# Optimization experiments

Measured on AMD Instinct MI355X. Metric: run time of the kernel, lower is better.

Reference implementation:

```python
import jax, jax.numpy as jnp
import numpy as np

B, N, K, DIMS, F_DIMS = 2, 32768, 16, 2, 32
DS, DH, DO = 32, 32, 32
DA = DS + DH                      # 64
CH = (DIMS + 1) * (1 + K) + DIMS  # 53
CONV_IN = DIMS + (1 + K) * DA     # 1090
CONV_OUT = (1 + K) * DO           # 544


def setup_inputs() -> dict:
    key = jax.random.key(0)
    ks = jax.random.split(key, 6)
    s = 0.05
    return {
        "pc": jax.random.normal(ks[0], (B, N, 1 + K, DIMS), jnp.float32),
        "feats": jax.random.normal(ks[1], (B, N, 1 + K, F_DIMS), jnp.float32),
        "W_mlp": jax.random.normal(ks[2], (CH, DS), jnp.float32) * s,
        "b_mlp": jnp.zeros((DS,), jnp.float32),
        "W_att": jax.random.normal(ks[3], (DA, DA), jnp.float32) * s,
        "b_att": jnp.zeros((DA,), jnp.float32),
        "W_conv": jax.random.normal(ks[4], (CONV_IN, CONV_OUT), jnp.float32) * s,
        "b_conv": jnp.zeros((CONV_OUT,), jnp.float32),
        "W_skip": jax.random.normal(ks[5], (DO + F_DIMS, DO), jnp.float32) * s,
        "b_skip": jnp.zeros((DO,), jnp.float32),
    }


def reference(pc, feats, W_mlp, b_mlp, W_att, b_att, W_conv, b_conv, W_skip, b_skip):
    # ---- LocSE: relative-position encoding ----
    # rpbn_i[b,n,j] = concat(pc[b,n,i] - pc[b,n,j], ||pc[b,n,j]||)
    norms = jnp.linalg.norm(pc, axis=-1, keepdims=True)          # (B,N,1+K,1)
    # diffs[b,n,j,i,:] = pc[b,n,i,:] - pc[b,n,j,:]
    diffs = pc[:, :, None, :, :] - pc[:, :, :, None, :]          # (B,N,1+K,1+K,dims)
    norms_b = jnp.broadcast_to(norms[:, :, :, None, :], diffs.shape[:-1] + (1,))
    blocks = jnp.concatenate([diffs, norms_b], axis=-1)          # (B,N,1+K,1+K,dims+1)
    blocks = blocks.reshape(pc.shape[:3] + ((1 + K) * (DIMS + 1),))
    rppe = jnp.concatenate([pc, blocks], axis=-1)                # (B,N,1+K,CH)
    r = jax.nn.relu(rppe @ W_mlp + b_mlp)                        # (B,N,1+K,DS)
    se = jnp.concatenate([r, feats], axis=-1)                    # (B,N,1+K,DA)

    # ---- attention pooling (softmax over channel axis) ----
    att = jax.nn.softmax(se @ W_att + b_att, axis=-1) * se       # (B,N,1+K,DA)
    reshaped = att.reshape(att.shape[0], att.shape[1], (1 + K) * DA)

    cat = jnp.concatenate([pc[:, :, 0], reshaped], axis=-1)      # (B,N,CONV_IN)
    res = jax.nn.relu(cat @ W_conv + b_conv)                     # (B,N,(1+K)*DO)
    res = res.reshape(res.shape[0], res.shape[1], 1 + K, DO)

    skip_in = jnp.concatenate([feats, res], axis=-1)             # (B,N,1+K,F+DO)
    skip = jax.nn.relu(skip_in @ W_skip + b_skip)                # (B,N,1+K,DO)
    return skip
```

## Files before the change

### kernel.cpp

```cpp
#include <hip/hip_runtime.h>
#include <hip/hip_bf16.h>
#include <cstdint>

#define KNB      17
#define CH       53
#define MP       16
#define BM       64
#define NTHR     512
#define NRT      17
#define SE_LD    72
#define CATW     1120
#define RES_LD   552
#define CHUNK_PTS 32768

#define NE_CONV  (35*34*512)
#define NE_MLP   (2*2*512)
#define NE_ATT   (2*4*512)
#define NE_SKIP  (2*2*512)
#define WS_MLP   (NE_CONV)
#define WS_ATT   (WS_MLP + NE_MLP)
#define WS_SKIP  (WS_ATT + NE_ATT)
#define WS_TOTAL (WS_SKIP + NE_SKIP)

typedef __bf16 bf16x8 __attribute__((ext_vector_type(8)));
typedef float  f32x4  __attribute__((ext_vector_type(4)));
typedef unsigned short u16x4 __attribute__((ext_vector_type(4)));
typedef unsigned short u16x8 __attribute__((ext_vector_type(8)));

__device__ __forceinline__ unsigned short f2b(float f) {
    union { __bf16 h; unsigned short u; } v; v.h = (__bf16)f; return v.u;
}
__device__ __forceinline__ float b2f(unsigned short b) {
    union { unsigned u; float f; } v; v.u = ((unsigned)b) << 16;
    return v.f;
}
__device__ __forceinline__ void gload_lds16(const void* g, void* l) {
    __builtin_amdgcn_global_load_lds(
        (const __attribute__((address_space(1))) unsigned int*)g,
        (__attribute__((address_space(3))) unsigned int*)l, 16, 0, 0);
}

__global__ void seac_prep(const float* __restrict__ Wmlp, const float* __restrict__ Watt,
                          const float* __restrict__ Wconv, const float* __restrict__ Wskip,
                          unsigned short* __restrict__ ws)
{
    int i = blockIdx.x * 256 + threadIdx.x;
    if (i >= WS_TOTAL) return;
    float v;
    if (i < WS_MLP) {
        int idx = i;
        int jj = idx & 7, l = (idx >> 3) & 63, t = idx >> 9;
        int nt = t % 34, ks = t / 34;
        int k = 32*ks + 8*(l >> 4) + jj;
        int o = 16*nt + (l & 15);
        int ok;
        if (k < 1088)       ok = k + 2;
        else if (k == 1088) ok = 0;
        else if (k == 1089) ok = 1;
        else                ok = -1;
        v = (ok >= 0) ? Wconv[ok*544 + o] : 0.f;
    } else if (i < WS_ATT) {
        int idx = i - WS_MLP;
        int jj = idx & 7, l = (idx >> 3) & 63, t = idx >> 9;
        int nt = t & 1, ks = t >> 1;
        int k = 32*ks + 8*(l >> 4) + jj;
        int o = 16*nt + (l & 15);
        v = (k < CH) ? Wmlp[k*32 + o] : 0.f;
    } else if (i < WS_SKIP) {
        int idx = i - WS_ATT;
        int jj = idx & 7, l = (idx >> 3) & 63, t = idx >> 9;
        int nt = t & 3, ks = t >> 2;
        int k = 32*ks + 8*(l >> 4) + jj;
        int o = 16*nt + (l & 15);
        v = Watt[k*64 + o];
    } else {
        int idx = i - WS_SKIP;
        int jj = idx & 7, l = (idx >> 3) & 63, t = idx >> 9;
        int nt = t & 1, ks = t >> 1;
        int k = 32*ks + 8*(l >> 4) + jj;
        int o = 16*nt + (l & 15);
        v = Wskip[k*32 + o];
    }
    ws[i] = f2b(v);
}

__global__ __launch_bounds__(NTHR, 6) void seac_locse(
    const float* __restrict__ pc, const float* __restrict__ feats,
    const float* __restrict__ bmlp, const float* __restrict__ batt,
    const unsigned short* __restrict__ ws, unsigned short* __restrict__ catg,
    int pt0)
{
    __shared__ unsigned short se_l[272 * SE_LD];
    __shared__ float pcl[MP][KNB][2];
    __shared__ float bmlp_l[32];
    __shared__ float batt_l[64];

    const int tid  = threadIdx.x;
    const int w    = tid >> 6;
    const int l    = tid & 63;
    const int g    = l >> 4;
    const int c15  = l & 15;
    const long pbase = (long)pt0 + (long)blockIdx.x * MP;
    const bf16x8* wsB8 = (const bf16x8*)ws;

    if (tid < MP*KNB) {
        int p = tid / KNB, i = tid - p*KNB;
        float x = pc[(pbase + p)*(KNB*2) + 2*i];
        float y = pc[(pbase + p)*(KNB*2) + 2*i + 1];
        pcl[p][i][0] = x; pcl[p][i][1] = y;
    }
    for (int q = tid; q < MP*544/4; q += NTHR) {
        float4 f = *(const float4*)&feats[pbase*544 + 4*q];
        int e0 = 4*q; int p = e0 / 544; int rem = e0 - 544*p;
        int j = rem >> 5, c = rem & 31;
        u16x4 u; u[0] = f2b(f.x); u[1] = f2b(f.y); u[2] = f2b(f.z); u[3] = f2b(f.w);
        *(u16x4*)&se_l[(p*KNB + j)*SE_LD + 32 + c] = u;
    }
    if (tid < 32)                     bmlp_l[tid]      = bmlp[tid];
    else if (tid >= 64 && tid < 128)  batt_l[tid-64]   = batt[tid-64];
    __syncthreads();

    {
        bf16x8 Bm[2][2];
        #pragma unroll
        for (int ks = 0; ks < 2; ++ks)
            #pragma unroll
            for (int nt = 0; nt < 2; ++nt)
                Bm[ks][nt] = wsB8[(WS_MLP >> 3) + (ks*2 + nt)*64 + l];
        float bch[2][4];
        #pragma unroll
        for (int nt = 0; nt < 2; ++nt)
            #pragma unroll
            for (int r = 0; r < 4; ++r) bch[nt][r] = bmlp_l[16*nt + 4*g + r];

        for (int mt = w; mt < NRT; mt += 8) {
            int row = 16*mt + c15;
            int p = row / KNB, j = row - p*KNB;
            float pjx = pcl[p][j][0], pjy = pcl[p][j][1];
            float nj = sqrtf(pjx*pjx + pjy*pjy);
            f32x4 acc0 = {0.f,0.f,0.f,0.f}, acc1 = {0.f,0.f,0.f,0.f};
            #pragma unroll
            for (int ks = 0; ks < 2; ++ks) {
                union { unsigned short u[8]; bf16x8 v; } a;
                #pragma unroll
                for (int jj = 0; jj < 8; ++jj) {
                    int k = 32*ks + 8*g + jj;
                    float vv;
                    if (k == 0) vv = pjx;
                    else if (k == 1) vv = pjy;
                    else if (k < CH) {
                        int kk = k - 2, ii = kk/3, t3 = kk - 3*ii;
                        vv = (t3 == 0) ? (pcl[p][ii][0] - pjx)
                           : (t3 == 1) ? (pcl[p][ii][1] - pjy) : nj;
                    } else vv = 0.f;
                    a.u[jj] = f2b(vv);
                }
                acc0 = __builtin_amdgcn_mfma_f32_16x16x32_bf16(Bm[ks][0], a.v, acc0, 0, 0, 0);
                acc1 = __builtin_amdgcn_mfma_f32_16x16x32_bf16(Bm[ks][1], a.v, acc1, 0, 0, 0);
            }
            u16x4 o0, o1;
            #pragma unroll
            for (int r = 0; r < 4; ++r) {
                o0[r] = f2b(fmaxf(acc0[r] + bch[0][r], 0.f));
                o1[r] = f2b(fmaxf(acc1[r] + bch[1][r], 0.f));
            }
            *(u16x4*)&se_l[row*SE_LD + 4*g]      = o0;
            *(u16x4*)&se_l[row*SE_LD + 16 + 4*g] = o1;
        }
    }
    __syncthreads();

    {
        bf16x8 Ba[2][4];
        #pragma unroll
        for (int ks = 0; ks < 2; ++ks)
            #pragma unroll
            for (int nt = 0; nt < 4; ++nt)
                Ba[ks][nt] = wsB8[(WS_ATT >> 3) + (ks*4 + nt)*64 + l];
        float bch[16];
        #pragma unroll
        for (int nt = 0; nt < 4; ++nt)
            #pragma unroll
            for (int r = 0; r < 4; ++r) bch[4*nt+r] = batt_l[16*nt + 4*g + r];

        for (int mt = w; mt < NRT; mt += 8) {
            int row = 16*mt + c15;
            bf16x8 b0 = *(const bf16x8*)&se_l[row*SE_LD + 8*g];
            bf16x8 b1 = *(const bf16x8*)&se_l[row*SE_LD + 32 + 8*g];
            f32x4 acc[4];
            #pragma unroll
            for (int nt = 0; nt < 4; ++nt) {
                f32x4 z = {0.f,0.f,0.f,0.f};
                acc[nt] = __builtin_amdgcn_mfma_f32_16x16x32_bf16(Ba[0][nt], b0, z,       0, 0, 0);
                acc[nt] = __builtin_amdgcn_mfma_f32_16x16x32_bf16(Ba[1][nt], b1, acc[nt], 0, 0, 0);
            }
            float vv[16];
            #pragma unroll
            for (int nt = 0; nt < 4; ++nt)
                #pragma unroll
                for (int r = 0; r < 4; ++r) vv[4*nt+r] = acc[nt][r] + bch[4*nt+r];
            float m = vv[0];
            #pragma unroll
            for (int i = 1; i < 16; ++i) m = fmaxf(m, vv[i]);
            m = fmaxf(m, __shfl_xor(m, 16)); m = fmaxf(m, __shfl_xor(m, 32));
            float s = 0.f;
            #pragma unroll
            for (int i = 0; i < 16; ++i) { vv[i] = __expf(vv[i] - m); s += vv[i]; }
            s += __shfl_xor(s, 16); s += __shfl_xor(s, 32);
            float inv = 1.f / s;
            #pragma unroll
            for (int nt = 0; nt < 4; ++nt) {
                u16x4 sv = *(const u16x4*)&se_l[row*SE_LD + 16*nt + 4*g];
                u16x4 ov;
                #pragma unroll
                for (int r = 0; r < 4; ++r) ov[r] = f2b(vv[4*nt+r]*inv * b2f(sv[r]));
                *(u16x4*)&se_l[row*SE_LD + 16*nt + 4*g] = ov;
            }
        }
    }
    __syncthreads();

    for (int c = tid; c < MP*140; c += NTHR) {
        int p = c / 140, rem = c - 140*p;
        int e = 8*rem;
        u16x8 v;
        if (e < 1088) {
            int row = p*KNB + (e >> 6), col = e & 63;
            v = *(const u16x8*)&se_l[row*SE_LD + col];
        } else {
            #pragma unroll
            for (int q = 0; q < 8; ++q) v[q] = 0;
            if (e == 1088) { v[0] = f2b(pcl[p][0][0]); v[1] = f2b(pcl[p][0][1]); }
        }
        *(u16x8*)&catg[(pbase + p)*CATW + e] = v;
    }
}

__global__ __launch_bounds__(NTHR, 4) void seac_conv(
    const unsigned short* __restrict__ catg, const float* __restrict__ feats,
    const float* __restrict__ bconv, const float* __restrict__ bskip,
    const unsigned short* __restrict__ ws, float* __restrict__ out, int pt0)
{
    __shared__ unsigned short astage[2][BM][32];
    __shared__ unsigned short res_l[BM * RES_LD];
    __shared__ float bconv_l[544];

    const int tid  = threadIdx.x;
    const int w    = tid >> 6;
    const int l    = tid & 63;
    const int g    = l >> 4;
    const int c15  = l & 15;
    const long pbase = (long)pt0 + (long)blockIdx.x * BM;
    const bf16x8* wsB8 = (const bf16x8*)ws;

    for (int i = tid; i < 544; i += NTHR) bconv_l[i] = bconv[i];

    if (tid < 256) {
        const unsigned short* gsrc = &catg[(pbase + (tid >> 2))*CATW + 8*(tid & 3)];
        gload_lds16(gsrc, &astage[0][16*(tid >> 6)][0]);
    }
    asm volatile("s_waitcnt vmcnt(0)" ::: "memory");
    __syncthreads();

    f32x4 acc[4][5];
    #pragma unroll
    for (int mt = 0; mt < 4; ++mt)
        #pragma unroll
        for (int t = 0; t < 5; ++t) { f32x4 z = {0.f,0.f,0.f,0.f}; acc[mt][t] = z; }

    int cur = 0;
    for (int ks = 0; ks < 35; ++ks) {
        if (ks + 1 < 35 && tid < 256) {
            const unsigned short* gsrc = &catg[(pbase + (tid >> 2))*CATW + 32*(ks+1) + 8*(tid & 3)];
            gload_lds16(gsrc, &astage[cur ^ 1][16*(tid >> 6)][0]);
        }
        bf16x8 a[4];
        #pragma unroll
        for (int mt = 0; mt < 4; ++mt)
            a[mt] = *(const bf16x8*)&astage[cur][16*mt + c15][8*g];
        #pragma unroll
        for (int t = 0; t < 5; ++t) {
            int nt = w + 8*t;
            if (nt < 34) {
                bf16x8 b = wsB8[(ks*34 + nt)*64 + l];
                #pragma unroll
                for (int mt = 0; mt < 4; ++mt)
                    acc[mt][t] = __builtin_amdgcn_mfma_f32_16x16x32_bf16(a[mt], b, acc[mt][t], 0, 0, 0);
            }
        }
        asm volatile("s_waitcnt vmcnt(0)" ::: "memory");
        __syncthreads();
        cur ^= 1;
    }

    #pragma unroll
    for (int t = 0; t < 5; ++t) {
        int nt = w + 8*t;
        if (nt < 34) {
            float bc = bconv_l[16*nt + c15];
            #pragma unroll
            for (int mt = 0; mt < 4; ++mt)
                #pragma unroll
                for (int r = 0; r < 4; ++r)
                    res_l[(16*mt + 4*g + r)*RES_LD + 16*nt + c15] =
                        f2b(fmaxf(acc[mt][t][r] + bc, 0.f));
        }
    }
    __syncthreads();

    {
        bf16x8 Bs[2][2];
        #pragma unroll
        for (int ks = 0; ks < 2; ++ks)
            #pragma unroll
            for (int nt = 0; nt < 2; ++nt)
                Bs[ks][nt] = wsB8[(WS_SKIP >> 3) + (ks*2 + nt)*64 + l];
        float4 bs0 = *(const float4*)&bskip[4*g];
        float4 bs1 = *(const float4*)&bskip[16 + 4*g];

        for (int tt = 0; tt < 9; ++tt) {
            int mt2 = w + 8*tt;
            if (mt2 < 68) {
                int rr = 16*mt2 + c15;
                int pp = rr / 17, jn = rr - 17*pp;
                float4 f0 = *(const float4*)&feats[(pbase*KNB + rr)*32 + 8*g];
                float4 f1 = *(const float4*)&feats[(pbase*KNB + rr)*32 + 8*g + 4];
                union { unsigned short u[8]; bf16x8 v; } af;
                af.u[0]=f2b(f0.x); af.u[1]=f2b(f0.y); af.u[2]=f2b(f0.z); af.u[3]=f2b(f0.w);
                af.u[4]=f2b(f1.x); af.u[5]=f2b(f1.y); af.u[6]=f2b(f1.z); af.u[7]=f2b(f1.w);
                bf16x8 br = *(const bf16x8*)&res_l[pp*RES_LD + 32*jn + 8*g];
                f32x4 z = {0.f,0.f,0.f,0.f};
                f32x4 a0 = __builtin_amdgcn_mfma_f32_16x16x32_bf16(Bs[0][0], af.v, z, 0, 0, 0);
                a0       = __builtin_amdgcn_mfma_f32_16x16x32_bf16(Bs[1][0], br,   a0, 0, 0, 0);
                f32x4 a1 = __builtin_amdgcn_mfma_f32_16x16x32_bf16(Bs[0][1], af.v, z, 0, 0, 0);
                a1       = __builtin_amdgcn_mfma_f32_16x16x32_bf16(Bs[1][1], br,   a1, 0, 0, 0);
                float4 o0, o1;
                o0.x = fmaxf(a0[0] + bs0.x, 0.f); o0.y = fmaxf(a0[1] + bs0.y, 0.f);
                o0.z = fmaxf(a0[2] + bs0.z, 0.f); o0.w = fmaxf(a0[3] + bs0.w, 0.f);
                o1.x = fmaxf(a1[0] + bs1.x, 0.f); o1.y = fmaxf(a1[1] + bs1.y, 0.f);
                o1.z = fmaxf(a1[2] + bs1.z, 0.f); o1.w = fmaxf(a1[3] + bs1.w, 0.f);
                long orow = pbase*KNB + rr;
                *(float4*)&out[orow*32 + 4*g]      = o0;
                *(float4*)&out[orow*32 + 16 + 4*g] = o1;
            }
        }
    }
}

extern "C" void kernel_launch(void* const* d_in, const int* in_sizes, int n_in,
                              void* d_out, int out_size, void* d_ws, size_t ws_size,
                              hipStream_t stream)
{
    const float* pc    = (const float*)d_in[0];
    const float* feats = (const float*)d_in[1];
    const float* Wmlp  = (const float*)d_in[2];
    const float* bmlp  = (const float*)d_in[3];
    const float* Watt  = (const float*)d_in[4];
    const float* batt  = (const float*)d_in[5];
    const float* Wconv = (const float*)d_in[6];
    const float* bconv = (const float*)d_in[7];
    const float* Wskip = (const float*)d_in[8];
    const float* bskip = (const float*)d_in[9];
    float* out = (float*)d_out;
    unsigned short* ws16 = (unsigned short*)d_ws;

    int npts = in_sizes[0] / (KNB*2);

    size_t frag_bytes = (size_t)WS_TOTAL * 2;
    size_t cat_off    = (frag_bytes + 255) & ~(size_t)255;
    unsigned short* catg = (unsigned short*)((char*)d_ws + cat_off);
    size_t avail = (ws_size > cat_off) ? (ws_size - cat_off) : 0;
    long maxpts = (long)(avail / (CATW * 2));
    long chunk  = (maxpts / BM) * BM;
    if (chunk > CHUNK_PTS) chunk = CHUNK_PTS;
    if (chunk > npts) chunk = npts;
    if (chunk < BM)   chunk = BM;

    int prep_blocks = (WS_TOTAL + 255) / 256;
    hipLaunchKernelGGL(seac_prep, dim3(prep_blocks), dim3(256), 0, stream,
                       Wmlp, Watt, Wconv, Wskip, ws16);

    for (long base = 0; base < npts; base += chunk) {
        long c = npts - base; if (c > chunk) c = chunk;
        hipLaunchKernelGGL(seac_locse, dim3((int)(c / MP)), dim3(NTHR), 0, stream,
                           pc, feats, bmlp, batt, ws16, catg, (int)base);
        hipLaunchKernelGGL(seac_conv, dim3((int)(c / BM)), dim3(NTHR), 0, stream,
                           catg, feats, bconv, bskip, ws16, out, (int)base);
    }
}
```

Baseline: 308.6 us.

## Split skip projection out of conv kernel into separate kernel via global buffer

Moves the skip-connection MFMA stage out of the conv kernel. The conv kernel now writes its ReLU result to a global bf16 buffer, and a new lightweight 256-thread kernel reads feats and that buffer to compute the skip output. The aim is to drop the serialized tail work and feats loads from the heavy conv kernel so it finishes sooner, and to let the skip pass run with full parallelism. In exchange it adds an extra global write and read of the intermediate, a third launch per chunk, and a smaller chunk size because of the extra workspace.

```diff
diff --git a/kernel.cpp b/kernel.cpp
--- a/kernel.cpp
+++ b/kernel.cpp
@@ -236,10 +236,11 @@
     }
 }
 
-__global__ __launch_bounds__(NTHR, 4) void seac_conv(
-    const unsigned short* __restrict__ catg, const float* __restrict__ feats,
-    const float* __restrict__ bconv, const float* __restrict__ bskip,
-    const unsigned short* __restrict__ ws, float* __restrict__ out, int pt0)
+__global__ __launch_bounds__(NTHR, 4) void seac_convk(
+    const unsigned short* __restrict__ catg,
+    const float* __restrict__ bconv,
+    const unsigned short* __restrict__ ws, unsigned short* __restrict__ resg,
+    int pt0)
 {
     __shared__ unsigned short astage[2][BM][32];
     __shared__ unsigned short res_l[BM * RES_LD];
@@ -251,6 +252,7 @@
     const int g    = l >> 4;
     const int c15  = l & 15;
     const long pbase = (long)pt0 + (long)blockIdx.x * BM;
+    const long crel  = (long)blockIdx.x * BM;
     const bf16x8* wsB8 = (const bf16x8*)ws;
 
     for (int i = tid; i < 544; i += NTHR) bconv_l[i] = bconv[i];
@@ -308,43 +310,55 @@
     }
     __syncthreads();
 
-    {
-        bf16x8 Bs[2][2];
-        #pragma unroll
-        for (int ks = 0; ks < 2; ++ks)
-            #pragma unroll
-            for (int nt = 0; nt < 2; ++nt)
-                Bs[ks][nt] = wsB8[(WS_SKIP >> 3) + (ks*2 + nt)*64 + l];
-        float4 bs0 = *(const float4*)&bskip[4*g];
-        float4 bs1 = *(const float4*)&bskip[16 + 4*g];
-
-        for (int tt = 0; tt < 9; ++tt) {
-            int mt2 = w + 8*tt;
-            if (mt2 < 68) {
-                int rr = 16*mt2 + c15;
-                int pp = rr / 17, jn = rr - 17*pp;
-                float4 f0 = *(const float4*)&feats[(pbase*KNB + rr)*32 + 8*g];
-                float4 f1 = *(const float4*)&feats[(pbase*KNB + rr)*32 + 8*g + 4];
-                union { unsigned short u[8]; bf16x8 v; } af;
-                af.u[0]=f2b(f0.x); af.u[1]=f2b(f0.y); af.u[2]=f2b(f0.z); af.u[3]=f2b(f0.w);
-                af.u[4]=f2b(f1.x); af.u[5]=f2b(f1.y); af.u[6]=f2b(f1.z); af.u[7]=f2b(f1.w);
-                bf16x8 br = *(const bf16x8*)&res_l[pp*RES_LD + 32*jn + 8*g];
-                f32x4 z = {0.f,0.f,0.f,0.f};
-                f32x4 a0 = __builtin_amdgcn_mfma_f32_16x16x32_bf16(Bs[0][0], af.v, z, 0, 0, 0);
-                a0       = __builtin_amdgcn_mfma_f32_16x16x32_bf16(Bs[1][0], br,   a0, 0, 0, 0);
-                f32x4 a1 = __builtin_amdgcn_mfma_f32_16x16x32_bf16(Bs[0][1], af.v, z, 0, 0, 0);
-                a1       = __builtin_amdgcn_mfma_f32_16x16x32_bf16(Bs[1][1], br,   a1, 0, 0, 0);
-                float4 o0, o1;
-                o0.x = fmaxf(a0[0] + bs0.x, 0.f); o0.y = fmaxf(a0[1] + bs0.y, 0.f);
-                o0.z = fmaxf(a0[2] + bs0.z, 0.f); o0.w = fmaxf(a0[3] + bs0.w, 0.f);
-                o1.x = fmaxf(a1[0] + bs1.x, 0.f); o1.y = fmaxf(a1[1] + bs1.y, 0.f);
-                o1.z = fmaxf(a1[2] + bs1.z, 0.f); o1.w = fmaxf(a1[3] + bs1.w, 0.f);
-                long orow = pbase*KNB + rr;
-                *(float4*)&out[orow*32 + 4*g]      = o0;
-                *(float4*)&out[orow*32 + 16 + 4*g] = o1;
-            }
-        }
-    }
+    for (int idx = tid; idx < BM*68; idx += NTHR) {
+        int p = idx / 68, q = idx - 68*p;
+        u16x8 v = *(const u16x8*)&res_l[p*RES_LD + 8*q];
+        *(u16x8*)&resg[(crel + p)*544 + 8*q] = v;
+    }
+}
+
+__global__ __launch_bounds__(256) void seac_skip(
+    const float* __restrict__ feats, const unsigned short* __restrict__ resg,
+    const float* __restrict__ bskip, const unsigned short* __restrict__ ws,
+    float* __restrict__ out, long row0)
+{
+    const int tid = threadIdx.x;
+    const int w   = tid >> 6;
+    const int l   = tid & 63;
+    const int g   = l >> 4;
+    const int c15 = l & 15;
+    const bf16x8* wsB8 = (const bf16x8*)ws;
+
+    bf16x8 Bs[2][2];
+    #pragma unroll
+    for (int ks = 0; ks < 2; ++ks)
+        #pragma unroll
+        for (int nt = 0; nt < 2; ++nt)
+            Bs[ks][nt] = wsB8[(WS_SKIP >> 3) + (ks*2 + nt)*64 + l];
+    float4 bs0 = *(const float4*)&bskip[4*g];
+    float4 bs1 = *(const float4*)&bskip[16 + 4*g];
+
+    long lr = ((long)blockIdx.x*4 + w)*16 + c15;
+    long rr = row0 + lr;
+    float4 f0 = *(const float4*)&feats[rr*32 + 8*g];
+    float4 f1 = *(const float4*)&feats[rr*32 + 8*g + 4];
+    union { unsigned short u[8]; bf16x8 v; } af;
+    af.u[0]=f2b(f0.x); af.u[1]=f2b(f0.y); af.u[2]=f2b(f0.z); af.u[3]=f2b(f0.w);
+    af.u[4]=f2b(f1.x); af.u[5]=f2b(f1.y); af.u[6]=f2b(f1.z); af.u[7]=f2b(f1.w);
+    bf16x8 br = *(const bf16x8*)&resg[lr*32 + 8*g];
+
+    f32x4 z = {0.f,0.f,0.f,0.f};
+    f32x4 a0 = __builtin_amdgcn_mfma_f32_16x16x32_bf16(Bs[0][0], af.v, z, 0, 0, 0);
+    a0       = __builtin_amdgcn_mfma_f32_16x16x32_bf16(Bs[1][0], br,   a0, 0, 0, 0);
+    f32x4 a1 = __builtin_amdgcn_mfma_f32_16x16x32_bf16(Bs[0][1], af.v, z, 0, 0, 0);
+    a1       = __builtin_amdgcn_mfma_f32_16x16x32_bf16(Bs[1][1], br,   a1, 0, 0, 0);
+    float4 o0, o1;
+    o0.x = fmaxf(a0[0] + bs0.x, 0.f); o0.y = fmaxf(a0[1] + bs0.y, 0.f);
+    o0.z = fmaxf(a0[2] + bs0.z, 0.f); o0.w = fmaxf(a0[3] + bs0.w, 0.f);
+    o1.x = fmaxf(a1[0] + bs1.x, 0.f); o1.y = fmaxf(a1[1] + bs1.y, 0.f);
+    o1.z = fmaxf(a1[2] + bs1.z, 0.f); o1.w = fmaxf(a1[3] + bs1.w, 0.f);
+    *(float4*)&out[rr*32 + 4*g]      = o0;
+    *(float4*)&out[rr*32 + 16 + 4*g] = o1;
 }
 
 extern "C" void kernel_launch(void* const* d_in, const int* in_sizes, int n_in,
@@ -364,17 +378,18 @@
     float* out = (float*)d_out;
     unsigned short* ws16 = (unsigned short*)d_ws;
 
-    int npts = in_sizes[0] / (KNB*2);
+    long npts = in_sizes[0] / (KNB*2);
 
     size_t frag_bytes = (size_t)WS_TOTAL * 2;
     size_t cat_off    = (frag_bytes + 255) & ~(size_t)255;
-    unsigned short* catg = (unsigned short*)((char*)d_ws + cat_off);
     size_t avail = (ws_size > cat_off) ? (ws_size - cat_off) : 0;
-    long maxpts = (long)(avail / (CATW * 2));
+    long maxpts = (long)(avail / (CATW*2 + 544*2));
     long chunk  = (maxpts / BM) * BM;
     if (chunk > CHUNK_PTS) chunk = CHUNK_PTS;
     if (chunk > npts) chunk = npts;
     if (chunk < BM)   chunk = BM;
+    unsigned short* catg = (unsigned short*)((char*)d_ws + cat_off);
+    unsigned short* resg = catg + (size_t)chunk * CATW;
 
     int prep_blocks = (WS_TOTAL + 255) / 256;
     hipLaunchKernelGGL(seac_prep, dim3(prep_blocks), dim3(256), 0, stream,
@@ -384,7 +399,10 @@
         long c = npts - base; if (c > chunk) c = chunk;
         hipLaunchKernelGGL(seac_locse, dim3((int)(c / MP)), dim3(NTHR), 0, stream,
                            pc, feats, bmlp, batt, ws16, catg, (int)base);
-        hipLaunchKernelGGL(seac_conv, dim3((int)(c / BM)), dim3(NTHR), 0, stream,
-                           catg, feats, bconv, bskip, ws16, out, (int)base);
-    }
-}
+        hipLaunchKernelGGL(seac_convk, dim3((int)(c / BM)), dim3(NTHR), 0, stream,
+                           catg, bconv, ws16, resg, (int)base);
+        long rows = c * KNB;
+        hipLaunchKernelGGL(seac_skip, dim3((int)(rows / 64)), dim3(256), 0, stream,
+                           feats, resg, bskip, ws16, out, base * KNB);
+    }
+}
```

Result: slower. 327.2 us (+6.0%).
